# Kernel tuning notes

Hardware: AMD Instinct MI355X
Metric: run time of the kernel (lower is better)

Reference implementation:

```python
import jax, jax.numpy as jnp
import numpy as np

B, T, D = 8, 2048, 128


def setup_inputs() -> dict:
    key = jax.random.key(0)
    kq, kk, kv = jax.random.split(key, 3)
    q = jax.random.normal(kq, (B, T, D), dtype=jnp.float32)
    k = jax.random.normal(kk, (B, T, D), dtype=jnp.float32)
    v = jax.random.normal(kv, (B, T, D), dtype=jnp.float32)
    # causal mask, broadcast over batch; 0 -> masked
    mask = jnp.tril(jnp.ones((T, T), dtype=jnp.int32))[None, :, :]
    mode = jnp.float32(0.5)  # learnable scalar parameter (init 0.5)
    return {"q": q, "k": k, "v": v, "mask": mask, "mode": mode}


def reference(q, k, v, mask, mode):
    scale = D ** (-0.5)
    # meson score: -(Q K^T) * scale
    meson = -jnp.einsum("btd,bsd->bts", q, k) * scale
    # baryon score: Q against K with feature dim rolled by 1
    k_perm = jnp.roll(k, shift=1, axis=-1)
    baryon = jnp.einsum("btd,bsd->bts", q, k_perm) * scale
    alpha = jax.nn.sigmoid(mode)
    attn = alpha * meson + (1.0 - alpha) * baryon
    attn = jnp.where(mask == 0, -jnp.inf, attn)
    attn = jax.nn.softmax(attn, axis=-1)
    return jnp.einsum("bts,bsd->btd", attn, v)
```

## Files before the change

kernel.cpp:

```cpp
#include <hip/hip_runtime.h>
#include <hip/hip_bf16.h>
#include <cstdint>
#include <cstddef>


typedef __attribute__((ext_vector_type(8))) short short8;
typedef __attribute__((ext_vector_type(4))) float f32x4;

#define T_DIM 2048
#define D_DIM 128
#define B_DIM 8
#define SEGT 4
#define POSLOTS_PER_B 56
#define MLSLOTS_PER_B 72

__device__ __forceinline__ unsigned short f2bf(float f) {
  unsigned u = __builtin_bit_cast(unsigned, f);
  u += 0x7FFFu + ((u >> 16) & 1u);
  return (unsigned short)(u >> 16);
}
__device__ __forceinline__ float bf2f(unsigned short u) {
  return __uint_as_float(((unsigned)u) << 16);
}
__device__ __forceinline__ void gload_lds16(const void* g, void* l) {
  __builtin_amdgcn_global_load_lds(
      (const __attribute__((address_space(1))) unsigned int*)g,
      (__attribute__((address_space(3))) unsigned int*)l, 16, 0, 0);
}

__global__ __launch_bounds__(256) void prep_all(
    const float* __restrict__ q, const float* __restrict__ k, const float* __restrict__ v,
    const float* __restrict__ modep,
    unsigned short* __restrict__ qbf, unsigned short* __restrict__ kbf,
    unsigned short* __restrict__ vt)
{
  __shared__ unsigned short tile[64 * 136];
  const int b = blockIdx.x, s0 = blockIdx.y * 64;
  const int tid = threadIdx.x;
  const float alpha = 1.f / (1.f + __expf(-modep[0]));
  const float scale = 0.08838834764831845f;
  const float ca = -alpha * scale, cb = (1.f - alpha) * scale;

#pragma unroll
  for (int u = 0; u < 4; ++u) {
    int c = u * 256 + tid;
    int r = c >> 4, c8 = c & 15;
    size_t row = (size_t)b * T_DIM + s0 + r;
    float4 ka = *(const float4*)(k + row * D_DIM + c8 * 8);
    float4 kb2 = *(const float4*)(k + row * D_DIM + c8 * 8 + 4);
    short8 ko = { (short)f2bf(ka.x), (short)f2bf(ka.y), (short)f2bf(ka.z), (short)f2bf(ka.w),
                  (short)f2bf(kb2.x), (short)f2bf(kb2.y), (short)f2bf(kb2.z), (short)f2bf(kb2.w) };
    *(short8*)(kbf + row * D_DIM + c8 * 8) = ko;
    const float* qr = q + row * D_DIM;
    float e[9];
    float4 f0 = *(const float4*)(qr + c8 * 8);
    float4 f1 = *(const float4*)(qr + c8 * 8 + 4);
    e[0] = f0.x; e[1] = f0.y; e[2] = f0.z; e[3] = f0.w;
    e[4] = f1.x; e[5] = f1.y; e[6] = f1.z; e[7] = f1.w;
    e[8] = qr[(c8 * 8 + 8) & 127];
    short8 qo;
#pragma unroll
    for (int j = 0; j < 8; ++j) qo[j] = (short)f2bf(ca * e[j] + cb * e[j + 1]);
    *(short8*)(qbf + row * D_DIM + c8 * 8) = qo;
    float4 va = *(const float4*)(v + row * D_DIM + c8 * 8);
    float4 vb2 = *(const float4*)(v + row * D_DIM + c8 * 8 + 4);
    short8 vo = { (short)f2bf(va.x), (short)f2bf(va.y), (short)f2bf(va.z), (short)f2bf(va.w),
                  (short)f2bf(vb2.x), (short)f2bf(vb2.y), (short)f2bf(vb2.z), (short)f2bf(vb2.w) };
    *(short8*)(tile + r * 136 + c8 * 8) = vo;
  }
  __syncthreads();
#pragma unroll
  for (int u = 0; u < 8; ++u) {
    int c = u * 256 + tid;
    int d = c >> 4, sq = c & 15;
    ushort4 o = { tile[(sq * 4 + 0) * 136 + d], tile[(sq * 4 + 1) * 136 + d],
                  tile[(sq * 4 + 2) * 136 + d], tile[(sq * 4 + 3) * 136 + d] };
    *(ushort4*)(vt + ((size_t)b * D_DIM + d) * T_DIM + s0 + sq * 4) = o;
  }
}

__global__ __launch_bounds__(256, 2) void attn_kernel(
    const unsigned short* __restrict__ qbf, const unsigned short* __restrict__ kbf,
    const unsigned short* __restrict__ vt, float* __restrict__ out,
    unsigned short* __restrict__ po, float* __restrict__ ml)
{
  __shared__ uint4 smem4[4608];
  char* smem = (char*)smem4;
  const int tid = threadIdx.x;
  const int w = tid >> 6, lane = tid & 63;
  const int t16 = lane & 15, g = lane >> 4;
  const int b = blockIdx.x;
  const int c = blockIdx.y;
  const int s = blockIdx.z;
  const int nt = 2 * c + 2;
  const int nseg = (c + 2) >> 1;
  if (s >= nseg) return;
  const int t0 = s * SEGT;
  const int t1 = min(nt, t0 + SEGT);
  const int qb = c * 128 + w * 32;

  char* pw = smem + 65536 + w * 2048;
  const unsigned short* kbase = kbf + (size_t)b * T_DIM * D_DIM;
  const unsigned short* vbase = vt + (size_t)b * D_DIM * T_DIM;

  short8 qf[2][4];
#pragma unroll
  for (int mt = 0; mt < 2; ++mt) {
    const unsigned short* qr = qbf + ((size_t)b * T_DIM + qb + mt * 16 + t16) * D_DIM + g * 8;
#pragma unroll
    for (int dd = 0; dd < 4; ++dd) qf[mt][dd] = *(const short8*)(qr + dd * 32);
  }

  f32x4 acc[2][8];
#pragma unroll
  for (int mt = 0; mt < 2; ++mt)
#pragma unroll
    for (int dt = 0; dt < 8; ++dt) acc[mt][dt] = (f32x4){0.f, 0.f, 0.f, 0.f};
  float mrun[2][4], lsum[2][4];
#pragma unroll
  for (int mt = 0; mt < 2; ++mt)
#pragma unroll
    for (int r = 0; r < 4; ++r) { mrun[mt][r] = -1e30f; lsum[mt][r] = 0.f; }

  auto stage = [&](int cur, int kt) {
    const int kv0 = kt * 64;
    char* kb = smem + cur * 16384;
    char* vb = smem + 32768 + cur * 16384;
#pragma unroll
    for (int u = 0; u < 4; ++u) {
      int s_loc = w * 16 + u * 4 + (lane >> 4);
      int slot = (lane & 15) ^ (s_loc & 7);
      gload_lds16(kbase + (size_t)(kv0 + s_loc) * D_DIM + slot * 8,
                  kb + w * 4096 + u * 1024);
    }
#pragma unroll
    for (int u = 0; u < 4; ++u) {
      int d_loc = w * 32 + u * 8 + (lane >> 3);
      int vslot = (lane & 7) ^ (d_loc & 7);
      gload_lds16(vbase + (size_t)d_loc * T_DIM + kv0 + vslot * 8,
                  vb + w * 4096 + u * 1024);
    }
  };

  stage(0, t0);
  __syncthreads();
  int cur = 0;

  for (int kt = t0; kt < t1; ++kt) {
    if (kt + 1 < t1) stage(cur ^ 1, kt + 1);
    const int kv0 = kt * 64;

    if (kv0 <= qb + 31) {
      char* kb = smem + cur * 16384;
      char* vb = smem + 32768 + cur * 16384;

      f32x4 sj[2][4];
#pragma unroll
      for (int jt = 0; jt < 4; ++jt) {
        int srow = jt * 16 + t16;
        int rb = srow * 256, swz = (srow & 7) << 4;
        f32x4 s0 = (f32x4){0.f, 0.f, 0.f, 0.f};
        f32x4 s1 = (f32x4){0.f, 0.f, 0.f, 0.f};
#pragma unroll
        for (int dd = 0; dd < 4; ++dd) {
          short8 kf = *(const short8*)(kb + ((rb + dd * 64 + g * 16) ^ swz));
          s0 = __builtin_amdgcn_mfma_f32_16x16x32_bf16(qf[0][dd], kf, s0, 0, 0, 0);
          s1 = __builtin_amdgcn_mfma_f32_16x16x32_bf16(qf[1][dd], kf, s1, 0, 0, 0);
        }
        sj[0][jt] = s0; sj[1][jt] = s1;
      }

      if (kv0 + 63 > qb) {
#pragma unroll
        for (int mt = 0; mt < 2; ++mt)
#pragma unroll
          for (int jt = 0; jt < 4; ++jt) {
            int sg = kv0 + jt * 16 + t16;
#pragma unroll
            for (int r = 0; r < 4; ++r) {
              int tg = qb + mt * 16 + 4 * g + r;
              if (sg > tg) sj[mt][jt][r] = -1e30f;
            }
          }
      }

      float lm[2][4];
      int ok = 1;
#pragma unroll
      for (int mt = 0; mt < 2; ++mt)
#pragma unroll
        for (int r = 0; r < 4; ++r) {
          lm[mt][r] = fmaxf(fmaxf(sj[mt][0][r], sj[mt][1][r]),
                            fmaxf(sj[mt][2][r], sj[mt][3][r]));
          ok &= (lm[mt][r] <= mrun[mt][r] + 8.0f);
        }
      if (!__all(ok)) {
#pragma unroll
        for (int mt = 0; mt < 2; ++mt) {
          float tm[4];
#pragma unroll
          for (int r = 0; r < 4; ++r) tm[r] = lm[mt][r];
#pragma unroll
          for (int r = 0; r < 4; ++r) {
            tm[r] = fmaxf(tm[r], __shfl_xor(tm[r], 1));
            tm[r] = fmaxf(tm[r], __shfl_xor(tm[r], 2));
            tm[r] = fmaxf(tm[r], __shfl_xor(tm[r], 4));
            tm[r] = fmaxf(tm[r], __shfl_xor(tm[r], 8));
          }
#pragma unroll
          for (int r = 0; r < 4; ++r) {
            float mnew = fmaxf(mrun[mt][r], tm[r]);
            float corr = __expf(mrun[mt][r] - mnew);
            mrun[mt][r] = mnew;
            lsum[mt][r] *= corr;
#pragma unroll
            for (int dt = 0; dt < 8; ++dt) acc[mt][dt][r] *= corr;
          }
        }
      }

#pragma unroll
      for (int mt = 0; mt < 2; ++mt) {
        float ls[4] = {0.f, 0.f, 0.f, 0.f};
#pragma unroll
        for (int jt = 0; jt < 4; ++jt)
#pragma unroll
          for (int r = 0; r < 4; ++r) {
            float p = __expf(sj[mt][jt][r] - mrun[mt][r]);
            sj[mt][jt][r] = p;
            ls[r] += p;
          }
#pragma unroll
        for (int r = 0; r < 4; ++r) lsum[mt][r] += ls[r];
#pragma unroll
        for (int jt = 0; jt < 4; ++jt)
#pragma unroll
          for (int r = 0; r < 4; ++r) {
            int rloc = 4 * g + r;
            *(unsigned short*)(pw + rloc * 128 + ((2 * (jt * 16 + t16)) ^ ((rloc & 7) << 4))) =
                f2bf(sj[mt][jt][r]);
          }
#pragma unroll
        for (int k0 = 0; k0 < 2; ++k0) {
          short8 pf = *(const short8*)(pw + t16 * 128 + ((k0 * 64 + g * 16) ^ ((t16 & 7) << 4)));
#pragma unroll
          for (int dt = 0; dt < 8; ++dt) {
            int d = dt * 16 + t16;
            short8 vf = *(const short8*)(vb + d * 128 + (((k0 * 4 + g) << 4) ^ ((d & 7) << 4)));
            acc[mt][dt] = __builtin_amdgcn_mfma_f32_16x16x32_bf16(pf, vf, acc[mt][dt], 0, 0, 0);
          }
        }
      }
    }

    __syncthreads();
    cur ^= 1;
  }

  float lred[2][4];
#pragma unroll
  for (int mt = 0; mt < 2; ++mt)
#pragma unroll
    for (int r = 0; r < 4; ++r) {
      float v0 = lsum[mt][r];
      v0 += __shfl_xor(v0, 1);
      v0 += __shfl_xor(v0, 2);
      v0 += __shfl_xor(v0, 4);
      v0 += __shfl_xor(v0, 8);
      lred[mt][r] = v0;
    }

  if (nseg == 1) {
#pragma unroll
    for (int mt = 0; mt < 2; ++mt)
#pragma unroll
      for (int r = 0; r < 4; ++r) {
        float inv = 1.0f / lred[mt][r];
#pragma unroll
        for (int dt = 0; dt < 8; ++dt)
          out[((size_t)b * T_DIM + qb + mt * 16 + 4 * g + r) * D_DIM + dt * 16 + t16] =
              acc[mt][dt][r] * inv;
      }
  } else {
    int pofs = 0;
    for (int cc = 0; cc < c; ++cc) pofs += ((cc + 2) >> 1) - 1;
    if (s == 0) {
#pragma unroll
      for (int mt = 0; mt < 2; ++mt)
#pragma unroll
        for (int r = 0; r < 4; ++r)
#pragma unroll
          for (int dt = 0; dt < 8; ++dt)
            out[((size_t)b * T_DIM + qb + mt * 16 + 4 * g + r) * D_DIM + dt * 16 + t16] =
                acc[mt][dt][r];
    } else {
      unsigned short* pob = po + ((size_t)b * POSLOTS_PER_B + pofs + (s - 1)) * 16384;
#pragma unroll
      for (int mt = 0; mt < 2; ++mt)
#pragma unroll
        for (int r = 0; r < 4; ++r) {
          int rb = w * 32 + mt * 16 + 4 * g + r;
#pragma unroll
          for (int dt = 0; dt < 8; ++dt)
            pob[rb * 128 + dt * 16 + t16] = f2bf(acc[mt][dt][r]);
        }
    }
    if (t16 == 0) {
      const size_t mlslot = (size_t)b * MLSLOTS_PER_B + pofs + c + s;
#pragma unroll
      for (int mt = 0; mt < 2; ++mt)
#pragma unroll
        for (int r = 0; r < 4; ++r) {
          int rb = w * 32 + mt * 16 + 4 * g + r;
          ml[mlslot * 256 + rb] = mrun[mt][r];
          ml[mlslot * 256 + 128 + rb] = lred[mt][r];
        }
    }
  }
}

__global__ __launch_bounds__(256) void combine_kernel(
    const unsigned short* __restrict__ po, const float* __restrict__ ml,
    float* __restrict__ out)
{
  const int tid = threadIdx.x;
  const int b = blockIdx.x;
  const int c = 2 + (int)blockIdx.y;
  const int nseg = (c + 2) >> 1;
  int pofs = 0;
  for (int cc = 0; cc < c; ++cc) pofs += ((cc + 2) >> 1) - 1;
  const size_t mlbase = (size_t)b * MLSLOTS_PER_B + pofs + c;
  const size_t pobase = (size_t)b * POSLOTS_PER_B + pofs;

  __shared__ float wgt[128][8];
  if (tid < 128) {
    float M = -1e30f;
    for (int s = 0; s < nseg; ++s)
      M = fmaxf(M, ml[(mlbase + s) * 256 + tid]);
    float L = 0.f;
    for (int s = 0; s < nseg; ++s) {
      float e = __expf(ml[(mlbase + s) * 256 + tid] - M);
      wgt[tid][s] = e;
      L += e * ml[(mlbase + s) * 256 + 128 + tid];
    }
    float invL = 1.f / L;
    for (int s = 0; s < nseg; ++s) wgt[tid][s] *= invL;
  }
  __syncthreads();

#pragma unroll
  for (int it = 0; it < 8; ++it) {
    int vid = it * 256 + tid;
    int r = vid >> 4, ch = vid & 15;
    float* op = out + ((size_t)b * T_DIM + c * 128 + r) * D_DIM + ch * 8;
    float4 a0 = *(const float4*)op;
    float4 a1 = *(const float4*)(op + 4);
    float w0 = wgt[r][0];
    float o[8] = { w0 * a0.x, w0 * a0.y, w0 * a0.z, w0 * a0.w,
                   w0 * a1.x, w0 * a1.y, w0 * a1.z, w0 * a1.w };
    for (int s = 1; s < nseg; ++s) {
      short8 pv = *(const short8*)(po + (pobase + s - 1) * 16384 + r * 128 + ch * 8);
      float ws = wgt[r][s];
#pragma unroll
      for (int j = 0; j < 8; ++j) o[j] += ws * bf2f((unsigned short)pv[j]);
    }
    *(float4*)op = (float4){o[0], o[1], o[2], o[3]};
    *(float4*)(op + 4) = (float4){o[4], o[5], o[6], o[7]};
  }
}

extern "C" void kernel_launch(void* const* d_in, const int* in_sizes, int n_in,
                              void* d_out, int out_size, void* d_ws, size_t ws_size,
                              hipStream_t stream) {
  const float* q = (const float*)d_in[0];
  const float* k = (const float*)d_in[1];
  const float* v = (const float*)d_in[2];
  const float* mode = (const float*)d_in[4];
  float* out = (float*)d_out;

  char* ws = (char*)d_ws;
  unsigned short* qbf = (unsigned short*)(ws);
  unsigned short* kbf = (unsigned short*)(ws + 4194304);
  unsigned short* vtb = (unsigned short*)(ws + 8388608);
  unsigned short* po  = (unsigned short*)(ws + 12582912);
  float*          ml  = (float*)(ws + 27262976);

  prep_all<<<dim3(B_DIM, T_DIM / 64), 256, 0, stream>>>(q, k, v, mode, qbf, kbf, vtb);
  attn_kernel<<<dim3(B_DIM, 16, 8), 256, 0, stream>>>(qbf, kbf, vtb, out, po, ml);
  combine_kernel<<<dim3(B_DIM, 14), 256, 0, stream>>>(po, ml, out);
}
```

Before: 61.61 us.

## Retile causal attention to 64-query blocks with 32-key tiles and exp2 softmax

The attention kernel now uses 128-thread blocks that each own 64 queries, and it streams 32-key tiles, so the grid has twice as many query chunks and smaller LDS buffers. Causal masking is applied only on the diagonal tile. Chunks are launched in reverse order so the heaviest ones start first, and the split-K segments, partial buffers and combine kernel are resized to match. The softmax uses exp2 with log2(e) folded into the Q prescale, and the lazy-rescale threshold is adjusted to that base. The aim is better load balance and occupancy on a causal workload, at the cost of less K/V reuse per block and more partial-result traffic.

```diff
diff --git a/kernel.cpp b/kernel.cpp
--- a/kernel.cpp
+++ b/kernel.cpp
@@ -10,9 +10,10 @@
 #define T_DIM 2048
 #define D_DIM 128
 #define B_DIM 8
-#define SEGT 4
-#define POSLOTS_PER_B 56
-#define MLSLOTS_PER_B 72
+#define SEGT 8
+#define POSLOTS_PER_B 112
+#define MLSLOTS_PER_B 144
+#define LOG2E 1.4426950408889634f
 
 __device__ __forceinline__ unsigned short f2bf(float f) {
   unsigned u = __builtin_bit_cast(unsigned, f);
@@ -39,7 +40,7 @@
   const int tid = threadIdx.x;
   const float alpha = 1.f / (1.f + __expf(-modep[0]));
   const float scale = 0.08838834764831845f;
-  const float ca = -alpha * scale, cb = (1.f - alpha) * scale;
+  const float ca = -alpha * scale * LOG2E, cb = (1.f - alpha) * scale * LOG2E;
 
 #pragma unroll
   for (int u = 0; u < 4; ++u) {
@@ -79,34 +80,34 @@
   }
 }
 
-__global__ __launch_bounds__(256, 2) void attn_kernel(
+__global__ __launch_bounds__(128, 2) void attn_kernel(
     const unsigned short* __restrict__ qbf, const unsigned short* __restrict__ kbf,
     const unsigned short* __restrict__ vt, float* __restrict__ out,
     unsigned short* __restrict__ po, float* __restrict__ ml)
 {
-  __shared__ uint4 smem4[4608];
+  __shared__ uint4 smem4[2304];
   char* smem = (char*)smem4;
   const int tid = threadIdx.x;
   const int w = tid >> 6, lane = tid & 63;
   const int t16 = lane & 15, g = lane >> 4;
   const int b = blockIdx.x;
-  const int c = blockIdx.y;
+  const int c = 31 - (int)blockIdx.y;
   const int s = blockIdx.z;
   const int nt = 2 * c + 2;
-  const int nseg = (c + 2) >> 1;
+  const int nseg = (c + 4) >> 2;
   if (s >= nseg) return;
   const int t0 = s * SEGT;
   const int t1 = min(nt, t0 + SEGT);
-  const int qb = c * 128 + w * 32;
-
-  char* pw = smem + 65536 + w * 2048;
+  const int qbw = c * 64 + w * 32;
+
+  char* pw = smem + 32768 + w * 2048;
   const unsigned short* kbase = kbf + (size_t)b * T_DIM * D_DIM;
   const unsigned short* vbase = vt + (size_t)b * D_DIM * T_DIM;
 
   short8 qf[2][4];
 #pragma unroll
   for (int mt = 0; mt < 2; ++mt) {
-    const unsigned short* qr = qbf + ((size_t)b * T_DIM + qb + mt * 16 + t16) * D_DIM + g * 8;
+    const unsigned short* qr = qbf + ((size_t)b * T_DIM + qbw + mt * 16 + t16) * D_DIM + g * 8;
 #pragma unroll
     for (int dd = 0; dd < 4; ++dd) qf[mt][dd] = *(const short8*)(qr + dd * 32);
   }
@@ -123,9 +124,9 @@
     for (int r = 0; r < 4; ++r) { mrun[mt][r] = -1e30f; lsum[mt][r] = 0.f; }
 
   auto stage = [&](int cur, int kt) {
-    const int kv0 = kt * 64;
-    char* kb = smem + cur * 16384;
-    char* vb = smem + 32768 + cur * 16384;
+    const int kv0 = kt * 32;
+    char* kb = smem + cur * 8192;
+    char* vb = smem + 16384 + cur * 8192;
 #pragma unroll
     for (int u = 0; u < 4; ++u) {
       int s_loc = w * 16 + u * 4 + (lane >> 4);
@@ -135,8 +136,8 @@
     }
 #pragma unroll
     for (int u = 0; u < 4; ++u) {
-      int d_loc = w * 32 + u * 8 + (lane >> 3);
-      int vslot = (lane & 7) ^ (d_loc & 7);
+      int d_loc = w * 64 + u * 16 + (lane >> 2);
+      int vslot = (lane & 3) ^ (d_loc & 3);
       gload_lds16(vbase + (size_t)d_loc * T_DIM + kv0 + vslot * 8,
                   vb + w * 4096 + u * 1024);
     }
@@ -148,15 +149,15 @@
 
   for (int kt = t0; kt < t1; ++kt) {
     if (kt + 1 < t1) stage(cur ^ 1, kt + 1);
-    const int kv0 = kt * 64;
-
-    if (kv0 <= qb + 31) {
-      char* kb = smem + cur * 16384;
-      char* vb = smem + 32768 + cur * 16384;
-
-      f32x4 sj[2][4];
-#pragma unroll
-      for (int jt = 0; jt < 4; ++jt) {
+    const int kv0 = kt * 32;
+
+    if (kv0 <= qbw + 31) {
+      char* kb = smem + cur * 8192;
+      char* vb = smem + 16384 + cur * 8192;
+
+      f32x4 sj[2][2];
+#pragma unroll
+      for (int jt = 0; jt < 2; ++jt) {
         int srow = jt * 16 + t16;
         int rb = srow * 256, swz = (srow & 7) << 4;
         f32x4 s0 = (f32x4){0.f, 0.f, 0.f, 0.f};
@@ -170,15 +171,15 @@
         sj[0][jt] = s0; sj[1][jt] = s1;
       }
 
-      if (kv0 + 63 > qb) {
+      if (kv0 == qbw) {
 #pragma unroll
         for (int mt = 0; mt < 2; ++mt)
 #pragma unroll
-          for (int jt = 0; jt < 4; ++jt) {
+          for (int jt = 0; jt < 2; ++jt) {
             int sg = kv0 + jt * 16 + t16;
 #pragma unroll
             for (int r = 0; r < 4; ++r) {
-              int tg = qb + mt * 16 + 4 * g + r;
+              int tg = qbw + mt * 16 + 4 * g + r;
               if (sg > tg) sj[mt][jt][r] = -1e30f;
             }
           }
@@ -190,66 +191,49 @@
       for (int mt = 0; mt < 2; ++mt)
 #pragma unroll
         for (int r = 0; r < 4; ++r) {
-          lm[mt][r] = fmaxf(fmaxf(sj[mt][0][r], sj[mt][1][r]),
-                            fmaxf(sj[mt][2][r], sj[mt][3][r]));
-          ok &= (lm[mt][r] <= mrun[mt][r] + 8.0f);
+          lm[mt][r] = fmaxf(sj[mt][0][r], sj[mt][1][r]);
+          ok &= (lm[mt][r] <= mrun[mt][r] + 11.0f);
         }
       if (!__all(ok)) {
 #pragma unroll
-        for (int mt = 0; mt < 2; ++mt) {
-          float tm[4];
-#pragma unroll
-          for (int r = 0; r < 4; ++r) tm[r] = lm[mt][r];
+        for (int mt = 0; mt < 2; ++mt)
 #pragma unroll
           for (int r = 0; r < 4; ++r) {
-            tm[r] = fmaxf(tm[r], __shfl_xor(tm[r], 1));
-            tm[r] = fmaxf(tm[r], __shfl_xor(tm[r], 2));
-            tm[r] = fmaxf(tm[r], __shfl_xor(tm[r], 4));
-            tm[r] = fmaxf(tm[r], __shfl_xor(tm[r], 8));
-          }
-#pragma unroll
-          for (int r = 0; r < 4; ++r) {
-            float mnew = fmaxf(mrun[mt][r], tm[r]);
-            float corr = __expf(mrun[mt][r] - mnew);
+            float tm = lm[mt][r];
+            tm = fmaxf(tm, __shfl_xor(tm, 1));
+            tm = fmaxf(tm, __shfl_xor(tm, 2));
+            tm = fmaxf(tm, __shfl_xor(tm, 4));
+            tm = fmaxf(tm, __shfl_xor(tm, 8));
+            float mnew = fmaxf(mrun[mt][r], tm);
+            float corr = exp2f(mrun[mt][r] - mnew);
             mrun[mt][r] = mnew;
             lsum[mt][r] *= corr;
 #pragma unroll
             for (int dt = 0; dt < 8; ++dt) acc[mt][dt][r] *= corr;
           }
-        }
-      }
-
-#pragma unroll
-      for (int mt = 0; mt < 2; ++mt) {
-        float ls[4] = {0.f, 0.f, 0.f, 0.f};
-#pragma unroll
-        for (int jt = 0; jt < 4; ++jt)
+      }
+
+#pragma unroll
+      for (int mt = 0; mt < 2; ++mt)
+#pragma unroll
+        for (int jt = 0; jt < 2; ++jt)
 #pragma unroll
           for (int r = 0; r < 4; ++r) {
-            float p = __expf(sj[mt][jt][r] - mrun[mt][r]);
-            sj[mt][jt][r] = p;
-            ls[r] += p;
+            float p = exp2f(sj[mt][jt][r] - mrun[mt][r]);
+            lsum[mt][r] += p;
+            int row = 4 * g + r;
+            *(unsigned short*)(pw + mt * 1024 + row * 64 +
+                               ((jt * 32 + t16 * 2) ^ ((row >> 2) << 4))) = f2bf(p);
           }
-#pragma unroll
-        for (int r = 0; r < 4; ++r) lsum[mt][r] += ls[r];
-#pragma unroll
-        for (int jt = 0; jt < 4; ++jt)
-#pragma unroll
-          for (int r = 0; r < 4; ++r) {
-            int rloc = 4 * g + r;
-            *(unsigned short*)(pw + rloc * 128 + ((2 * (jt * 16 + t16)) ^ ((rloc & 7) << 4))) =
-                f2bf(sj[mt][jt][r]);
-          }
-#pragma unroll
-        for (int k0 = 0; k0 < 2; ++k0) {
-          short8 pf = *(const short8*)(pw + t16 * 128 + ((k0 * 64 + g * 16) ^ ((t16 & 7) << 4)));
-#pragma unroll
-          for (int dt = 0; dt < 8; ++dt) {
-            int d = dt * 16 + t16;
-            short8 vf = *(const short8*)(vb + d * 128 + (((k0 * 4 + g) << 4) ^ ((d & 7) << 4)));
-            acc[mt][dt] = __builtin_amdgcn_mfma_f32_16x16x32_bf16(pf, vf, acc[mt][dt], 0, 0, 0);
-          }
-        }
+
+      short8 pf0 = *(const short8*)(pw + t16 * 64 + ((g * 16) ^ ((t16 >> 2) << 4)));
+      short8 pf1 = *(const short8*)(pw + 1024 + t16 * 64 + ((g * 16) ^ ((t16 >> 2) << 4)));
+#pragma unroll
+      for (int dt = 0; dt < 8; ++dt) {
+        int d = dt * 16 + t16;
+        short8 vf = *(const short8*)(vb + d * 64 + ((g * 16) ^ ((d & 3) << 4)));
+        acc[0][dt] = __builtin_amdgcn_mfma_f32_16x16x32_bf16(pf0, vf, acc[0][dt], 0, 0, 0);
+        acc[1][dt] = __builtin_amdgcn_mfma_f32_16x16x32_bf16(pf1, vf, acc[1][dt], 0, 0, 0);
       }
     }
 
@@ -278,12 +262,12 @@
         float inv = 1.0f / lred[mt][r];
 #pragma unroll
         for (int dt = 0; dt < 8; ++dt)
-          out[((size_t)b * T_DIM + qb + mt * 16 + 4 * g + r) * D_DIM + dt * 16 + t16] =
+          out[((size_t)b * T_DIM + qbw + mt * 16 + 4 * g + r) * D_DIM + dt * 16 + t16] =
               acc[mt][dt][r] * inv;
       }
   } else {
     int pofs = 0;
-    for (int cc = 0; cc < c; ++cc) pofs += ((cc + 2) >> 1) - 1;
+    for (int cc = 0; cc < c; ++cc) pofs += ((cc + 4) >> 2) - 1;
     if (s == 0) {
 #pragma unroll
       for (int mt = 0; mt < 2; ++mt)
@@ -291,10 +275,10 @@
         for (int r = 0; r < 4; ++r)
 #pragma unroll
           for (int dt = 0; dt < 8; ++dt)
-            out[((size_t)b * T_DIM + qb + mt * 16 + 4 * g + r) * D_DIM + dt * 16 + t16] =
+            out[((size_t)b * T_DIM + qbw + mt * 16 + 4 * g + r) * D_DIM + dt * 16 + t16] =
                 acc[mt][dt][r];
     } else {
-      unsigned short* pob = po + ((size_t)b * POSLOTS_PER_B + pofs + (s - 1)) * 16384;
+      unsigned short* pob = po + ((size_t)b * POSLOTS_PER_B + pofs + (s - 1)) * 8192;
 #pragma unroll
       for (int mt = 0; mt < 2; ++mt)
 #pragma unroll
@@ -312,8 +296,8 @@
 #pragma unroll
         for (int r = 0; r < 4; ++r) {
           int rb = w * 32 + mt * 16 + 4 * g + r;
-          ml[mlslot * 256 + rb] = mrun[mt][r];
-          ml[mlslot * 256 + 128 + rb] = lred[mt][r];
+          ml[mlslot * 128 + rb] = mrun[mt][r];
+          ml[mlslot * 128 + 64 + rb] = lred[mt][r];
         }
     }
   }
@@ -325,23 +309,23 @@
 {
   const int tid = threadIdx.x;
   const int b = blockIdx.x;
-  const int c = 2 + (int)blockIdx.y;
-  const int nseg = (c + 2) >> 1;
+  const int c = 4 + (int)blockIdx.y;
+  const int nseg = (c + 4) >> 2;
   int pofs = 0;
-  for (int cc = 0; cc < c; ++cc) pofs += ((cc + 2) >> 1) - 1;
+  for (int cc = 0; cc < c; ++cc) pofs += ((cc + 4) >> 2) - 1;
   const size_t mlbase = (size_t)b * MLSLOTS_PER_B + pofs + c;
   const size_t pobase = (size_t)b * POSLOTS_PER_B + pofs;
 
-  __shared__ float wgt[128][8];
-  if (tid < 128) {
+  __shared__ float wgt[64][8];
+  if (tid < 64) {
     float M = -1e30f;
     for (int s = 0; s < nseg; ++s)
-      M = fmaxf(M, ml[(mlbase + s) * 256 + tid]);
+      M = fmaxf(M, ml[(mlbase + s) * 128 + tid]);
     float L = 0.f;
     for (int s = 0; s < nseg; ++s) {
-      float e = __expf(ml[(mlbase + s) * 256 + tid] - M);
+      float e = exp2f(ml[(mlbase + s) * 128 + tid] - M);
       wgt[tid][s] = e;
-      L += e * ml[(mlbase + s) * 256 + 128 + tid];
+      L += e * ml[(mlbase + s) * 128 + 64 + tid];
     }
     float invL = 1.f / L;
     for (int s = 0; s < nseg; ++s) wgt[tid][s] *= invL;
@@ -349,17 +333,17 @@
   __syncthreads();
 
 #pragma unroll
-  for (int it = 0; it < 8; ++it) {
+  for (int it = 0; it < 4; ++it) {
     int vid = it * 256 + tid;
     int r = vid >> 4, ch = vid & 15;
-    float* op = out + ((size_t)b * T_DIM + c * 128 + r) * D_DIM + ch * 8;
+    float* op = out + ((size_t)b * T_DIM + c * 64 + r) * D_DIM + ch * 8;
     float4 a0 = *(const float4*)op;
     float4 a1 = *(const float4*)(op + 4);
     float w0 = wgt[r][0];
     float o[8] = { w0 * a0.x, w0 * a0.y, w0 * a0.z, w0 * a0.w,
                    w0 * a1.x, w0 * a1.y, w0 * a1.z, w0 * a1.w };
     for (int s = 1; s < nseg; ++s) {
-      short8 pv = *(const short8*)(po + (pobase + s - 1) * 16384 + r * 128 + ch * 8);
+      short8 pv = *(const short8*)(po + (pobase + s - 1) * 8192 + r * 128 + ch * 8);
       float ws = wgt[r][s];
 #pragma unroll
       for (int j = 0; j < 8; ++j) o[j] += ws * bf2f((unsigned short)pv[j]);
@@ -386,6 +370,6 @@
   float*          ml  = (float*)(ws + 27262976);
 
   prep_all<<<dim3(B_DIM, T_DIM / 64), 256, 0, stream>>>(q, k, v, mode, qbf, kbf, vtb);
-  attn_kernel<<<dim3(B_DIM, 16, 8), 256, 0, stream>>>(qbf, kbf, vtb, out, po, ml);
-  combine_kernel<<<dim3(B_DIM, 14), 256, 0, stream>>>(po, ml, out);
-}
+  attn_kernel<<<dim3(B_DIM, 32, SEGT), 128, 0, stream>>>(qbf, kbf, vtb, out, po, ml);
+  combine_kernel<<<dim3(B_DIM, 28), 256, 0, stream>>>(po, ml, out);
+}
```

Measured after the change: 56.85 us. 7.7% less time.
